# Optimization experiments

Hardware: AMD Instinct MI355X
Metric: run time of the kernel (lower is better)

Reference implementation:

```python
import jax, jax.numpy as jnp
import numpy as np

B, S, E, H, L = 8, 1024, 1024, 16, 2
D = E // H
EPS = 1e-5
THRESH = 0.5


def layer_norm(x, g, b):
    mu = x.mean(-1, keepdims=True)
    var = ((x - mu) ** 2).mean(-1, keepdims=True)
    return (x - mu) * jax.lax.rsqrt(var + EPS) * g + b


def mha(x, w_in, w_out):
    # x: [B,S,E]; w_in: [3E,E]; w_out: [E,E] (no biases, PyTorch MultiheadAttention bias=False)
    qkv = x @ w_in.T  # [B,S,3E]
    q, k, v = jnp.split(qkv, 3, axis=-1)
    q = q.reshape(q.shape[0], q.shape[1], H, D).transpose(0, 2, 1, 3)
    k = k.reshape(k.shape[0], k.shape[1], H, D).transpose(0, 2, 1, 3)
    v = v.reshape(v.shape[0], v.shape[1], H, D).transpose(0, 2, 1, 3)
    scores = jnp.einsum('bhqd,bhkd->bhqk', q, k) / jnp.sqrt(jnp.float32(D)).astype(x.dtype)
    attn = jax.nn.softmax(scores, axis=-1)
    out = jnp.einsum('bhqk,bhkd->bhqd', attn, v)
    out = out.transpose(0, 2, 1, 3).reshape(x.shape[0], x.shape[1], E)
    return out @ w_out.T


def thinking_layer(x, w_in, w_out, ffn1, ffn2, g1, b1, g2, b2):
    x = layer_norm(x + mha(x, w_in, w_out), g1, b1)
    h = jax.nn.gelu(x @ ffn1.T, approximate=False) @ ffn2.T
    return layer_norm(x + h, g2, b2)


def setup_inputs() -> dict:
    key = jax.random.key(0)
    ks = jax.random.split(key, 8)
    s = jnp.float32(0.02)
    return {
        'x': jax.random.normal(ks[0], (B, S, E), jnp.float32),
        'w_in': jax.random.normal(ks[1], (L, 3 * E, E), jnp.float32) * s,
        'w_out': jax.random.normal(ks[2], (L, E, E), jnp.float32) * s,
        'ffn_w1': jax.random.normal(ks[3], (L, 4 * E, E), jnp.float32) * s,
        'ffn_w2': jax.random.normal(ks[4], (L, E, 4 * E), jnp.float32) * s,
        'ln1_g': jnp.ones((L, E), jnp.float32),
        'ln1_b': jnp.zeros((L, E), jnp.float32),
        'ln2_g': jnp.ones((L, E), jnp.float32),
        'ln2_b': jnp.zeros((L, E), jnp.float32),
        'ce_w1': jax.random.normal(ks[5], (E // 4, E), jnp.float32) * s,
        'ce_b1': jnp.zeros((E // 4,), jnp.float32),
        'ce_w2': jax.random.normal(ks[6], (1, E // 4), jnp.float32) * s,
        'ce_b2': jnp.zeros((1,), jnp.float32),
        'fast_w': jax.random.normal(ks[7], (E, E), jnp.float32) * s,
    }


def reference(x, w_in, w_out, ffn_w1, ffn_w2, ln1_g, ln1_b, ln2_g, ln2_b,
              ce_w1, ce_b1, ce_w2, ce_b2, fast_w):
    # complexity estimator: mean-pool -> MLP -> logit per batch element
    pooled = x.mean(axis=1)                                   # [B,E]
    h = jax.nn.relu(pooled @ ce_w1.T + ce_b1)                 # [B,E/4]
    logits = (h @ ce_w2.T + ce_b2).squeeze(-1)                # [B]
    probs = jax.nn.sigmoid(logits)
    mode = (probs > THRESH)                                   # eval-mode deterministic routing

    # thinking path (System 2): L stacked attention+FFN layers
    t = x
    for i in range(L):
        t = thinking_layer(t, w_in[i], w_out[i], ffn_w1[i], ffn_w2[i],
                           ln1_g[i], ln1_b[i], ln2_g[i], ln2_b[i])

    # fast path (System 1)
    fast = jax.nn.gelu(x @ fast_w.T, approximate=False)

    out = jnp.where(mode[:, None, None], t, fast)
    mode_f = mode.astype(x.dtype)
    return out, probs, mode_f, mode_f.mean()
```

## Files before the change

kernel.cpp:

```cpp
#include <hip/hip_runtime.h>
#include <cstdint>
#include <cstddef>

#define Bsz 8
#define Ssz 1024
#define Esz 1024
#define Hn  16
#define Dh  64
#define OUT_PROBS 8388608
#define OUT_MODE  8388616
#define OUT_MEAN  8388624

typedef unsigned short u16;
typedef __attribute__((ext_vector_type(8))) __bf16 bf16x8;
typedef __attribute__((ext_vector_type(4))) float  floatx4;

__device__ __forceinline__ float bf2f(u16 u){ return __uint_as_float(((unsigned)u)<<16); }
__device__ __forceinline__ u16 f2bf(float f){
  unsigned u = __float_as_uint(f);
  u += 0x7fffu + ((u>>16)&1u);
  return (u16)(u>>16);
}
__device__ __forceinline__ void unpack2(unsigned u, float& lo, float& hi){
  lo = __uint_as_float(u<<16);
  hi = __uint_as_float(u & 0xffff0000u);
}
__device__ __forceinline__ unsigned pack2(float lo, float hi){
  return (unsigned)f2bf(lo) | ((unsigned)f2bf(hi)<<16);
}
__device__ __forceinline__ void async16(const void* g, void* l){
  __builtin_amdgcn_global_load_lds((const __attribute__((address_space(1))) void*)g,
                                   (__attribute__((address_space(3))) void*)l, 16, 0, 0);
}
__device__ __forceinline__ float gelu_exact(float x){
  return 0.5f*x*(1.0f + erff(x*0.70710678118654752f));
}

__global__ __launch_bounds__(256)
void f2b_kernel(const float* __restrict__ src, u16* __restrict__ dst, int n8)
{
  const int i = blockIdx.x*256 + threadIdx.x;
  if(i >= n8) return;
  float4 a = ((const float4*)src)[2*i];
  float4 b = ((const float4*)src)[2*i+1];
  uint4 w;
  w.x = pack2(a.x, a.y); w.y = pack2(a.z, a.w);
  w.z = pack2(b.x, b.y); w.w = pack2(b.z, b.w);
  ((uint4*)dst)[i] = w;
}

template<int EPI>
__global__ __launch_bounds__(256, 2)
void gemm_bt(const u16* __restrict__ A, const u16* __restrict__ W,
             void* __restrict__ Cv, const u16* __restrict__ R,
             int N, int K)
{
  __shared__ __align__(16) u16 As[128*32];
  __shared__ __align__(16) u16 Bs[128*32];

  const int tid  = threadIdx.x;
  const int wave = tid >> 6;
  const int lane = tid & 63;
  const int q    = lane >> 4;
  const int r16  = lane & 15;
  const int wm   = (wave >> 1) * 64;
  const int wn   = (wave & 1) * 64;
  const int m0   = blockIdx.x * 128;
  const int n0   = blockIdx.y * 128;

  floatx4 acc[4][4];
  #pragma unroll
  for(int i=0;i<4;i++)
    #pragma unroll
    for(int j=0;j<4;j++){ floatx4 z = {0.f,0.f,0.f,0.f}; acc[i][j] = z; }

  const int row0 = tid >> 2;
  const int kc   = (tid & 3) * 8;
  u16* lA0 = As + wave*512;          u16* lA1 = As + 2048 + wave*512;
  u16* lB0 = Bs + wave*512;          u16* lB1 = Bs + 2048 + wave*512;

  for(int k0 = 0; k0 < K; k0 += 32){
    __syncthreads();
    async16(A + (size_t)(m0 + row0     )*K + k0 + kc, lA0);
    async16(A + (size_t)(m0 + row0 + 64)*K + k0 + kc, lA1);
    async16(W + (size_t)(n0 + row0     )*K + k0 + kc, lB0);
    async16(W + (size_t)(n0 + row0 + 64)*K + k0 + kc, lB1);
    __syncthreads();

    bf16x8 af[4], bfr[4];
    #pragma unroll
    for(int i=0;i<4;i++){
      af[i]  = *(const bf16x8*)&As[(wm + i*16 + r16)*32 + q*8];
      bfr[i] = *(const bf16x8*)&Bs[(wn + i*16 + r16)*32 + q*8];
    }
    #pragma unroll
    for(int i=0;i<4;i++)
      #pragma unroll
      for(int j=0;j<4;j++)
        acc[i][j] = __builtin_amdgcn_mfma_f32_16x16x32_bf16(af[i], bfr[j], acc[i][j], 0, 0, 0);
  }

  #pragma unroll
  for(int i=0;i<4;i++){
    const int row = m0 + wm + i*16 + q*4;
    #pragma unroll
    for(int j=0;j<4;j++){
      const int col = n0 + wn + j*16 + r16;
      #pragma unroll
      for(int r=0;r<4;r++){
        float v = acc[i][j][r];
        const size_t idx = (size_t)(row + r)*N + col;
        if(EPI == 1) v += bf2f(R[idx]);
        if(EPI == 2 || EPI == 3) v = gelu_exact(v);
        if(EPI == 3) ((float*)Cv)[idx] = v;
        else         ((u16*)Cv)[idx] = f2bf(v);
      }
    }
  }
}

#define PSTR 136
__global__ __launch_bounds__(256, 2)
void attn_kernel(const u16* __restrict__ qkv, u16* __restrict__ out)
{
  __shared__ __align__(16) u16 Qs[2*64*32];
  __shared__ __align__(16) u16 Ks[2*128*32];
  __shared__ __align__(16) u16 Vt[64*PSTR];
  __shared__ __align__(16) u16 Ps[64*PSTR];
  __shared__ float lsump[2][64];

  const int tid = threadIdx.x;
  const int w   = tid >> 6;
  const int lane= tid & 63;
  const int q   = lane >> 4;
  const int r16 = lane & 15;

  const int qt = blockIdx.x >> 7;
  const int bh = blockIdx.x & 127;
  const int b  = bh >> 4;
  const int h  = bh & 15;
  const int q0 = qt * 64;

  const u16* qbase = qkv + (size_t)(b*Ssz)*3072;

  {
    const int r = tid >> 2;
    const int c = (tid & 3) * 8;
    #pragma unroll
    for(int half=0; half<2; half++)
      async16(qbase + (size_t)(q0 + r)*3072 + h*64 + half*32 + c,
              &Qs[half*2048 + w*512]);
  }

  const int wm = (w >> 1) * 32;
  const int wnS = (w & 1) * 64;
  const int wnO = (w & 1) * 32;

  floatx4 acc_o[2][2];
  #pragma unroll
  for(int i=0;i<2;i++)
    #pragma unroll
    for(int j=0;j<2;j++){ floatx4 z={0.f,0.f,0.f,0.f}; acc_o[i][j]=z; }
  float ps[2][4] = {{0.f,0.f,0.f,0.f},{0.f,0.f,0.f,0.f}};

  for(int ck=0; ck<8; ck++){
    const int k0 = ck*128;
    __syncthreads();
    {
      const int r = tid >> 2;
      const int c = (tid & 3) * 8;
      #pragma unroll
      for(int half=0; half<2; half++)
        #pragma unroll
        for(int g=0; g<2; g++)
          async16(qbase + (size_t)(k0 + g*64 + r)*3072 + 1024 + h*64 + half*32 + c,
                  &Ks[half*4096 + g*2048 + w*512]);
    }
    {
      const int r  = tid >> 1;
      const int cs = (tid & 1) * 32;
      const uint4* vp = (const uint4*)(qbase + (size_t)(k0 + r)*3072 + 2048 + h*64 + cs);
      #pragma unroll
      for(int u=0; u<4; u++){
        uint4 vv = vp[u];
        unsigned wd[4] = {vv.x, vv.y, vv.z, vv.w};
        #pragma unroll
        for(int p2=0; p2<4; p2++){
          const int d = cs + u*8 + p2*2;
          Vt[(size_t)d*PSTR + r]     = (u16)(wd[p2] & 0xffffu);
          Vt[(size_t)(d+1)*PSTR + r] = (u16)(wd[p2] >> 16);
        }
      }
    }
    __syncthreads();

    floatx4 accS[2][4];
    #pragma unroll
    for(int i=0;i<2;i++)
      #pragma unroll
      for(int j=0;j<4;j++){ floatx4 z={0.f,0.f,0.f,0.f}; accS[i][j]=z; }
    #pragma unroll
    for(int half=0; half<2; half++){
      bf16x8 af[2], bf[4];
      #pragma unroll
      for(int i=0;i<2;i++)
        af[i] = *(const bf16x8*)&Qs[half*2048 + (wm + i*16 + r16)*32 + q*8];
      #pragma unroll
      for(int j=0;j<4;j++)
        bf[j] = *(const bf16x8*)&Ks[half*4096 + (wnS + j*16 + r16)*32 + q*8];
      #pragma unroll
      for(int i=0;i<2;i++)
        #pragma unroll
        for(int j=0;j<4;j++)
          accS[i][j] = __builtin_amdgcn_mfma_f32_16x16x32_bf16(af[i], bf[j], accS[i][j], 0,0,0);
    }
    #pragma unroll
    for(int i=0;i<2;i++)
      #pragma unroll
      for(int j=0;j<4;j++)
        #pragma unroll
        for(int r=0;r<4;r++){
          const float p = __expf(accS[i][j][r] * 0.125f);
          ps[i][r] += p;
          Ps[(size_t)(wm + i*16 + q*4 + r)*PSTR + wnS + j*16 + r16] = f2bf(p);
        }
    __syncthreads();

    #pragma unroll
    for(int ks=0; ks<4; ks++){
      bf16x8 ap[2], bp[2];
      #pragma unroll
      for(int i=0;i<2;i++)
        ap[i] = *(const bf16x8*)&Ps[(size_t)(wm + i*16 + r16)*PSTR + ks*32 + q*8];
      #pragma unroll
      for(int j=0;j<2;j++)
        bp[j] = *(const bf16x8*)&Vt[(size_t)(wnO + j*16 + r16)*PSTR + ks*32 + q*8];
      #pragma unroll
      for(int i=0;i<2;i++)
        #pragma unroll
        for(int j=0;j<2;j++)
          acc_o[i][j] = __builtin_amdgcn_mfma_f32_16x16x32_bf16(ap[i], bp[j], acc_o[i][j], 0,0,0);
    }
  }

  #pragma unroll
  for(int i=0;i<2;i++)
    #pragma unroll
    for(int r=0;r<4;r++){
      float v = ps[i][r];
      v += __shfl_xor(v, 1, 64);
      v += __shfl_xor(v, 2, 64);
      v += __shfl_xor(v, 4, 64);
      v += __shfl_xor(v, 8, 64);
      ps[i][r] = v;
    }
  if(r16 == 0){
    #pragma unroll
    for(int i=0;i<2;i++)
      #pragma unroll
      for(int r=0;r<4;r++)
        lsump[w & 1][wm + i*16 + q*4 + r] = ps[i][r];
  }
  __syncthreads();

  #pragma unroll
  for(int i=0;i<2;i++)
    #pragma unroll
    for(int r=0;r<4;r++){
      const int row = wm + i*16 + q*4 + r;
      const float inv = 1.0f / (lsump[0][row] + lsump[1][row]);
      #pragma unroll
      for(int j=0;j<2;j++){
        const int col = h*64 + wnO + j*16 + r16;
        out[(size_t)(b*Ssz + q0 + row)*Esz + col] = f2bf(acc_o[i][j][r] * inv);
      }
    }
}

__global__ __launch_bounds__(256)
void ln_kernel(const u16* __restrict__ X, const float* __restrict__ G,
               const float* __restrict__ Bi, u16* __restrict__ Y)
{
  const int row = blockIdx.x;
  const int tid = threadIdx.x;
  const int wave = tid >> 6, lane = tid & 63;

  uint2 u = ((const uint2*)(X + (size_t)row*Esz))[tid];
  float x0,x1,x2,x3;
  unpack2(u.x, x0, x1); unpack2(u.y, x2, x3);
  float s  = x0+x1+x2+x3;
  float ss = x0*x0 + x1*x1 + x2*x2 + x3*x3;
  #pragma unroll
  for(int off=32; off; off>>=1){
    s  += __shfl_down(s,  off, 64);
    ss += __shfl_down(ss, off, 64);
  }
  __shared__ float rs[4], rss[4], bc[2];
  if(lane == 0){ rs[wave] = s; rss[wave] = ss; }
  __syncthreads();
  if(tid == 0){
    float S  = rs[0]+rs[1]+rs[2]+rs[3];
    float SS = rss[0]+rss[1]+rss[2]+rss[3];
    float mu  = S * (1.0f/1024.0f);
    float var = SS * (1.0f/1024.0f) - mu*mu;
    bc[0] = mu; bc[1] = 1.0f/sqrtf(var + 1e-5f);
  }
  __syncthreads();
  const float mu = bc[0], inv = bc[1];
  float4 g4 = ((const float4*)G)[tid];
  float4 b4 = ((const float4*)Bi)[tid];
  uint2 w;
  w.x = pack2((x0-mu)*inv*g4.x + b4.x, (x1-mu)*inv*g4.y + b4.y);
  w.y = pack2((x2-mu)*inv*g4.z + b4.z, (x3-mu)*inv*g4.w + b4.w);
  ((uint2*)(Y + (size_t)row*Esz))[tid] = w;
}

__global__ __launch_bounds__(256)
void pool1_kernel(const float* __restrict__ x, float* __restrict__ part)
{
  const int b = blockIdx.x, tc = blockIdx.y;
  const int e4 = threadIdx.x;
  const float* p = x + (size_t)(b*Ssz + tc*32)*Esz + e4*4;
  float4 s = {0.f,0.f,0.f,0.f};
  for(int t=0; t<32; t++){
    float4 v = *(const float4*)(p + (size_t)t*Esz);
    s.x += v.x; s.y += v.y; s.z += v.z; s.w += v.w;
  }
  ((float4*)(part + (size_t)(b*32 + tc)*Esz))[e4] = s;
}

__global__ void ce1_kernel(const float* __restrict__ part, const float* __restrict__ w1,
                           const float* __restrict__ b1, float* __restrict__ hbuf)
{
  __shared__ float pl[1024];
  const int b = blockIdx.x, n = threadIdx.x;
  for(int i = threadIdx.x; i < 1024; i += 256){
    float s = 0.f;
    for(int tc=0; tc<32; tc++) s += part[(size_t)(b*32 + tc)*Esz + i];
    pl[i] = s * (1.0f/1024.0f);
  }
  __syncthreads();
  const float* wr = w1 + (size_t)n*1024;
  float s = 0.f;
  for(int k=0; k<1024; k++) s += pl[k]*wr[k];
  s += b1[n];
  hbuf[b*256 + n] = fmaxf(s, 0.f);
}

__global__ void ce2_kernel(const float* __restrict__ hbuf, const float* __restrict__ w2,
                           const float* __restrict__ b2, float* __restrict__ modes,
                           float* __restrict__ outp)
{
  const int tid = threadIdx.x;
  const int b = tid >> 5, i = tid & 31;
  float s = 0.f;
  for(int k=i; k<256; k+=32) s += hbuf[b*256 + k] * w2[k];
  #pragma unroll
  for(int off=16; off; off>>=1) s += __shfl_down(s, off, 32);
  __shared__ float md[8];
  if(i == 0){
    const float logit = s + b2[0];
    const float prob = 1.0f/(1.0f + expf(-logit));
    const float m = prob > 0.5f ? 1.0f : 0.0f;
    modes[b] = m; md[b] = m;
    outp[OUT_PROBS + b] = prob;
    outp[OUT_MODE  + b] = m;
  }
  __syncthreads();
  if(tid == 0){
    float acc = 0.f;
    for(int k=0;k<8;k++) acc += md[k];
    outp[OUT_MEAN] = acc * 0.125f;
  }
}

__global__ __launch_bounds__(256)
void select_kernel(const float* __restrict__ modes, const u16* __restrict__ t,
                   float* __restrict__ outp)
{
  const int idx4 = blockIdx.x*256 + threadIdx.x;
  const int b = idx4 >> 18;
  if(modes[b] != 0.0f){
    uint2 u = ((const uint2*)t)[idx4];
    float4 f;
    unpack2(u.x, f.x, f.y); unpack2(u.y, f.z, f.w);
    ((float4*)outp)[idx4] = f;
  }
}

extern "C" void kernel_launch(void* const* d_in, const int* in_sizes, int n_in,
                              void* d_out, int out_size, void* d_ws, size_t ws_size,
                              hipStream_t stream)
{
  const float* x      = (const float*)d_in[0];
  const float* w_in   = (const float*)d_in[1];
  const float* w_out  = (const float*)d_in[2];
  const float* ffn_w1 = (const float*)d_in[3];
  const float* ffn_w2 = (const float*)d_in[4];
  const float* ln1_g  = (const float*)d_in[5];
  const float* ln1_b  = (const float*)d_in[6];
  const float* ln2_g  = (const float*)d_in[7];
  const float* ln2_b  = (const float*)d_in[8];
  const float* ce_w1  = (const float*)d_in[9];
  const float* ce_b1  = (const float*)d_in[10];
  const float* ce_w2  = (const float*)d_in[11];
  const float* ce_b2  = (const float*)d_in[12];
  const float* fast_w = (const float*)d_in[13];
  float* out = (float*)d_out;

  u16* x_bf     = (u16*)d_ws;
  u16* w_in_bf  = x_bf    + (size_t)8192*1024;
  u16* w_out_bf = w_in_bf + (size_t)2*3072*1024;
  u16* ffn1_bf  = w_out_bf+ (size_t)2*1024*1024;
  u16* ffn2_bf  = ffn1_bf + (size_t)2*4096*1024;
  u16* fast_bf  = ffn2_bf + (size_t)2*1024*4096;
  u16* big      = fast_bf + (size_t)1024*1024;
  u16* attn     = big     + (size_t)8192*4096;
  u16* resid    = attn    + (size_t)8192*1024;
  u16* bufA     = resid   + (size_t)8192*1024;
  u16* bufB     = bufA    + (size_t)8192*1024;
  float* part   = (float*)(bufB + (size_t)8192*1024);
  float* hbuf   = part + (size_t)8*32*1024;
  float* modes  = hbuf + 2048;
  const size_t need = (size_t)((char*)(modes + 8) - (char*)d_ws);
  if(ws_size < need) return;

  u16* qkv  = big;
  u16* hmid = big;

  f2b_kernel<<<4096, 256, 0, stream>>>(x,      x_bf,     8192*1024/8);
  f2b_kernel<<<3072, 256, 0, stream>>>(w_in,   w_in_bf,  2*3072*1024/8);
  f2b_kernel<<<1024, 256, 0, stream>>>(w_out,  w_out_bf, 2*1024*1024/8);
  f2b_kernel<<<4096, 256, 0, stream>>>(ffn_w1, ffn1_bf,  2*4096*1024/8);
  f2b_kernel<<<4096, 256, 0, stream>>>(ffn_w2, ffn2_bf,  2*4096*1024/8);
  f2b_kernel<<< 512, 256, 0, stream>>>(fast_w, fast_bf,  1024*1024/8);

  pool1_kernel<<<dim3(8,32), 256, 0, stream>>>(x, part);
  ce1_kernel<<<8, 256, 0, stream>>>(part, ce_w1, ce_b1, hbuf);
  ce2_kernel<<<1, 256, 0, stream>>>(hbuf, ce_w2, ce_b2, modes, out);

  const u16* t = x_bf;
  for(int l=0; l<2; l++){
    gemm_bt<0><<<dim3(64,24), 256, 0, stream>>>(t, w_in_bf + (size_t)l*3072*1024, qkv, nullptr, 3072, 1024);
    attn_kernel<<<2048, 256, 0, stream>>>(qkv, attn);
    gemm_bt<1><<<dim3(64, 8), 256, 0, stream>>>(attn, w_out_bf + (size_t)l*1024*1024, resid, t, 1024, 1024);
    ln_kernel<<<8192, 256, 0, stream>>>(resid, ln1_g + l*1024, ln1_b + l*1024, bufA);
    gemm_bt<2><<<dim3(64,32), 256, 0, stream>>>(bufA, ffn1_bf + (size_t)l*4096*1024, hmid, nullptr, 4096, 1024);
    gemm_bt<1><<<dim3(64, 8), 256, 0, stream>>>(hmid, ffn2_bf + (size_t)l*1024*4096, resid, bufA, 1024, 4096);
    ln_kernel<<<8192, 256, 0, stream>>>(resid, ln2_g + l*1024, ln2_b + l*1024, bufB);
    t = bufB;
  }

  gemm_bt<3><<<dim3(64, 8), 256, 0, stream>>>(x_bf, fast_bf, out, nullptr, 1024, 1024);
  select_kernel<<<8192, 256, 0, stream>>>(modes, bufB, out);
}
```

Before: 1.060 ms.

## Skip thinking or fast path per batch by mode, deepen GEMM K-tile, pack V transpose

Every thinking-path kernel (QKV, attention, out-proj, LN, FFN) now exits early for batch elements whose mode is 0, and the fast-path GEMM exits for batches whose mode is 1. This removes the discarded half of the work. The final LN writes fp32 straight into the output, so the select kernel goes away. The GEMM also loads 64 K per barrier pair (double the LDS), and the attention V transpose writes packed 32-bit words. Runtime now depends on how many batches take each route.

Result: faster. 958.7 us (-9.5%).

```diff
diff --git a/kernel.cpp b/kernel.cpp
--- a/kernel.cpp
+++ b/kernel.cpp
@@ -49,14 +49,20 @@
   ((uint4*)dst)[i] = w;
 }
 
-template<int EPI>
+template<int EPI, int SKIP>
 __global__ __launch_bounds__(256, 2)
 void gemm_bt(const u16* __restrict__ A, const u16* __restrict__ W,
              void* __restrict__ Cv, const u16* __restrict__ R,
-             int N, int K)
-{
-  __shared__ __align__(16) u16 As[128*32];
-  __shared__ __align__(16) u16 Bs[128*32];
+             const float* __restrict__ modes, int N, int K)
+{
+  const int m0 = blockIdx.x * 128;
+  if(SKIP == 1 && modes[m0 >> 10] == 0.0f) return;
+  if(SKIP == 2 && modes[m0 >> 10] != 0.0f) return;
+
+  __shared__ __align__(16) u16 AsLo[128*32];
+  __shared__ __align__(16) u16 AsHi[128*32];
+  __shared__ __align__(16) u16 BsLo[128*32];
+  __shared__ __align__(16) u16 BsHi[128*32];
 
   const int tid  = threadIdx.x;
   const int wave = tid >> 6;
@@ -65,7 +71,6 @@
   const int r16  = lane & 15;
   const int wm   = (wave >> 1) * 64;
   const int wn   = (wave & 1) * 64;
-  const int m0   = blockIdx.x * 128;
   const int n0   = blockIdx.y * 128;
 
   floatx4 acc[4][4];
@@ -76,28 +81,45 @@
 
   const int row0 = tid >> 2;
   const int kc   = (tid & 3) * 8;
-  u16* lA0 = As + wave*512;          u16* lA1 = As + 2048 + wave*512;
-  u16* lB0 = Bs + wave*512;          u16* lB1 = Bs + 2048 + wave*512;
-
-  for(int k0 = 0; k0 < K; k0 += 32){
+
+  for(int k0 = 0; k0 < K; k0 += 64){
     __syncthreads();
-    async16(A + (size_t)(m0 + row0     )*K + k0 + kc, lA0);
-    async16(A + (size_t)(m0 + row0 + 64)*K + k0 + kc, lA1);
-    async16(W + (size_t)(n0 + row0     )*K + k0 + kc, lB0);
-    async16(W + (size_t)(n0 + row0 + 64)*K + k0 + kc, lB1);
+    async16(A + (size_t)(m0 + row0     )*K + k0 + kc,      AsLo + wave*512);
+    async16(A + (size_t)(m0 + row0 + 64)*K + k0 + kc,      AsLo + 2048 + wave*512);
+    async16(A + (size_t)(m0 + row0     )*K + k0 + 32 + kc, AsHi + wave*512);
+    async16(A + (size_t)(m0 + row0 + 64)*K + k0 + 32 + kc, AsHi + 2048 + wave*512);
+    async16(W + (size_t)(n0 + row0     )*K + k0 + kc,      BsLo + wave*512);
+    async16(W + (size_t)(n0 + row0 + 64)*K + k0 + kc,      BsLo + 2048 + wave*512);
+    async16(W + (size_t)(n0 + row0     )*K + k0 + 32 + kc, BsHi + wave*512);
+    async16(W + (size_t)(n0 + row0 + 64)*K + k0 + 32 + kc, BsHi + 2048 + wave*512);
     __syncthreads();
 
-    bf16x8 af[4], bfr[4];
-    #pragma unroll
-    for(int i=0;i<4;i++){
-      af[i]  = *(const bf16x8*)&As[(wm + i*16 + r16)*32 + q*8];
-      bfr[i] = *(const bf16x8*)&Bs[(wn + i*16 + r16)*32 + q*8];
-    }
-    #pragma unroll
-    for(int i=0;i<4;i++)
-      #pragma unroll
-      for(int j=0;j<4;j++)
-        acc[i][j] = __builtin_amdgcn_mfma_f32_16x16x32_bf16(af[i], bfr[j], acc[i][j], 0, 0, 0);
+    {
+      bf16x8 af[4], bfr[4];
+      #pragma unroll
+      for(int i=0;i<4;i++){
+        af[i]  = *(const bf16x8*)&AsLo[(wm + i*16 + r16)*32 + q*8];
+        bfr[i] = *(const bf16x8*)&BsLo[(wn + i*16 + r16)*32 + q*8];
+      }
+      #pragma unroll
+      for(int i=0;i<4;i++)
+        #pragma unroll
+        for(int j=0;j<4;j++)
+          acc[i][j] = __builtin_amdgcn_mfma_f32_16x16x32_bf16(af[i], bfr[j], acc[i][j], 0, 0, 0);
+    }
+    {
+      bf16x8 af[4], bfr[4];
+      #pragma unroll
+      for(int i=0;i<4;i++){
+        af[i]  = *(const bf16x8*)&AsHi[(wm + i*16 + r16)*32 + q*8];
+        bfr[i] = *(const bf16x8*)&BsHi[(wn + i*16 + r16)*32 + q*8];
+      }
+      #pragma unroll
+      for(int i=0;i<4;i++)
+        #pragma unroll
+        for(int j=0;j<4;j++)
+          acc[i][j] = __builtin_amdgcn_mfma_f32_16x16x32_bf16(af[i], bfr[j], acc[i][j], 0, 0, 0);
+    }
   }
 
   #pragma unroll
@@ -121,8 +143,13 @@
 
 #define PSTR 136
 __global__ __launch_bounds__(256, 2)
-void attn_kernel(const u16* __restrict__ qkv, u16* __restrict__ out)
-{
+void attn_kernel(const u16* __restrict__ qkv, u16* __restrict__ out,
+                 const float* __restrict__ modes)
+{
+  const int bh = blockIdx.x & 127;
+  const int b  = bh >> 4;
+  if(modes[b] == 0.0f) return;
+
   __shared__ __align__(16) u16 Qs[2*64*32];
   __shared__ __align__(16) u16 Ks[2*128*32];
   __shared__ __align__(16) u16 Vt[64*PSTR];
@@ -136,8 +163,6 @@
   const int r16 = lane & 15;
 
   const int qt = blockIdx.x >> 7;
-  const int bh = blockIdx.x & 127;
-  const int b  = bh >> 4;
   const int h  = bh & 15;
   const int q0 = qt * 64;
 
@@ -152,7 +177,7 @@
               &Qs[half*2048 + w*512]);
   }
 
-  const int wm = (w >> 1) * 32;
+  const int wm  = (w >> 1) * 32;
   const int wnS = (w & 1) * 64;
   const int wnO = (w & 1) * 32;
 
@@ -177,19 +202,19 @@
                   &Ks[half*4096 + g*2048 + w*512]);
     }
     {
-      const int r  = tid >> 1;
-      const int cs = (tid & 1) * 32;
-      const uint4* vp = (const uint4*)(qbase + (size_t)(k0 + r)*3072 + 2048 + h*64 + cs);
-      #pragma unroll
-      for(int u=0; u<4; u++){
-        uint4 vv = vp[u];
-        unsigned wd[4] = {vv.x, vv.y, vv.z, vv.w};
-        #pragma unroll
-        for(int p2=0; p2<4; p2++){
-          const int d = cs + u*8 + p2*2;
-          Vt[(size_t)d*PSTR + r]     = (u16)(wd[p2] & 0xffffu);
-          Vt[(size_t)(d+1)*PSTR + r] = (u16)(wd[p2] >> 16);
-        }
+      const int kp = tid >> 2;
+      const int dg = tid & 3;
+      const uint4* v0 = (const uint4*)(qbase + (size_t)(k0 + 2*kp    )*3072 + 2048 + h*64 + dg*16);
+      const uint4* v1 = (const uint4*)(qbase + (size_t)(k0 + 2*kp + 1)*3072 + 2048 + h*64 + dg*16);
+      uint4 a0 = v0[0], a1 = v0[1], b0 = v1[0], b1 = v1[1];
+      unsigned wa[8] = {a0.x,a0.y,a0.z,a0.w,a1.x,a1.y,a1.z,a1.w};
+      unsigned wb[8] = {b0.x,b0.y,b0.z,b0.w,b1.x,b1.y,b1.z,b1.w};
+      unsigned* vt32 = (unsigned*)Vt;
+      #pragma unroll
+      for(int u=0; u<8; u++){
+        const int d = dg*16 + u*2;
+        vt32[(size_t)d*68 + kp]     = (wa[u] & 0xffffu) | (wb[u] << 16);
+        vt32[(size_t)(d+1)*68 + kp] = (wa[u] >> 16) | (wb[u] & 0xffff0000u);
       }
     }
     __syncthreads();
@@ -277,11 +302,14 @@
     }
 }
 
+template<int FIN>
 __global__ __launch_bounds__(256)
 void ln_kernel(const u16* __restrict__ X, const float* __restrict__ G,
-               const float* __restrict__ Bi, u16* __restrict__ Y)
+               const float* __restrict__ Bi, u16* __restrict__ Y,
+               const float* __restrict__ modes, float* __restrict__ outp)
 {
   const int row = blockIdx.x;
+  if(modes[row >> 10] == 0.0f) return;
   const int tid = threadIdx.x;
   const int wave = tid >> 6, lane = tid & 63;
 
@@ -309,10 +337,19 @@
   const float mu = bc[0], inv = bc[1];
   float4 g4 = ((const float4*)G)[tid];
   float4 b4 = ((const float4*)Bi)[tid];
-  uint2 w;
-  w.x = pack2((x0-mu)*inv*g4.x + b4.x, (x1-mu)*inv*g4.y + b4.y);
-  w.y = pack2((x2-mu)*inv*g4.z + b4.z, (x3-mu)*inv*g4.w + b4.w);
-  ((uint2*)(Y + (size_t)row*Esz))[tid] = w;
+  if(FIN){
+    float4 o;
+    o.x = (x0-mu)*inv*g4.x + b4.x;
+    o.y = (x1-mu)*inv*g4.y + b4.y;
+    o.z = (x2-mu)*inv*g4.z + b4.z;
+    o.w = (x3-mu)*inv*g4.w + b4.w;
+    ((float4*)(outp + (size_t)row*Esz))[tid] = o;
+  } else {
+    uint2 w;
+    w.x = pack2((x0-mu)*inv*g4.x + b4.x, (x1-mu)*inv*g4.y + b4.y);
+    w.y = pack2((x2-mu)*inv*g4.z + b4.z, (x3-mu)*inv*g4.w + b4.w);
+    ((uint2*)(Y + (size_t)row*Esz))[tid] = w;
+  }
 }
 
 __global__ __launch_bounds__(256)
@@ -371,20 +408,6 @@
     float acc = 0.f;
     for(int k=0;k<8;k++) acc += md[k];
     outp[OUT_MEAN] = acc * 0.125f;
-  }
-}
-
-__global__ __launch_bounds__(256)
-void select_kernel(const float* __restrict__ modes, const u16* __restrict__ t,
-                   float* __restrict__ outp)
-{
-  const int idx4 = blockIdx.x*256 + threadIdx.x;
-  const int b = idx4 >> 18;
-  if(modes[b] != 0.0f){
-    uint2 u = ((const uint2*)t)[idx4];
-    float4 f;
-    unpack2(u.x, f.x, f.y); unpack2(u.y, f.z, f.w);
-    ((float4*)outp)[idx4] = f;
   }
 }
 
@@ -441,16 +464,18 @@
 
   const u16* t = x_bf;
   for(int l=0; l<2; l++){
-    gemm_bt<0><<<dim3(64,24), 256, 0, stream>>>(t, w_in_bf + (size_t)l*3072*1024, qkv, nullptr, 3072, 1024);
-    attn_kernel<<<2048, 256, 0, stream>>>(qkv, attn);
-    gemm_bt<1><<<dim3(64, 8), 256, 0, stream>>>(attn, w_out_bf + (size_t)l*1024*1024, resid, t, 1024, 1024);
-    ln_kernel<<<8192, 256, 0, stream>>>(resid, ln1_g + l*1024, ln1_b + l*1024, bufA);
-    gemm_bt<2><<<dim3(64,32), 256, 0, stream>>>(bufA, ffn1_bf + (size_t)l*4096*1024, hmid, nullptr, 4096, 1024);
-    gemm_bt<1><<<dim3(64, 8), 256, 0, stream>>>(hmid, ffn2_bf + (size_t)l*1024*4096, resid, bufA, 1024, 4096);
-    ln_kernel<<<8192, 256, 0, stream>>>(resid, ln2_g + l*1024, ln2_b + l*1024, bufB);
+    gemm_bt<0,1><<<dim3(64,24), 256, 0, stream>>>(t, w_in_bf + (size_t)l*3072*1024, qkv, nullptr, modes, 3072, 1024);
+    attn_kernel<<<2048, 256, 0, stream>>>(qkv, attn, modes);
+    gemm_bt<1,1><<<dim3(64, 8), 256, 0, stream>>>(attn, w_out_bf + (size_t)l*1024*1024, resid, t, modes, 1024, 1024);
+    ln_kernel<0><<<8192, 256, 0, stream>>>(resid, ln1_g + l*1024, ln1_b + l*1024, bufA, modes, nullptr);
+    gemm_bt<2,1><<<dim3(64,32), 256, 0, stream>>>(bufA, ffn1_bf + (size_t)l*4096*1024, hmid, nullptr, modes, 4096, 1024);
+    gemm_bt<1,1><<<dim3(64, 8), 256, 0, stream>>>(hmid, ffn2_bf + (size_t)l*1024*4096, resid, bufA, modes, 1024, 4096);
+    if(l == 0)
+      ln_kernel<0><<<8192, 256, 0, stream>>>(resid, ln2_g + l*1024, ln2_b + l*1024, bufB, modes, nullptr);
+    else
+      ln_kernel<1><<<8192, 256, 0, stream>>>(resid, ln2_g + l*1024, ln2_b + l*1024, nullptr, modes, out);
     t = bufB;
   }
 
-  gemm_bt<3><<<dim3(64, 8), 256, 0, stream>>>(x_bf, fast_bf, out, nullptr, 1024, 1024);
-  select_kernel<<<8192, 256, 0, stream>>>(modes, bufB, out);
-}
+  gemm_bt<3,2><<<dim3(64, 8), 256, 0, stream>>>(x_bf, fast_bf, out, nullptr, modes, 1024, 1024);
+}
```
